# Kernel tuning notes

Measured on AMD Instinct MI355X. Metric: run time of the kernel, lower is better.

The kernel has to match this reference:

```python
import jax, jax.numpy as jnp
import numpy as np

B, N, D, NS, ITERS = 32, 2048, 512, 8, 3
EPS = 1e-8
SCALE = D ** -0.5
LN_EPS = 1e-5


def _ln(x, g, b):
    m = x.mean(-1, keepdims=True)
    v = ((x - m) ** 2).mean(-1, keepdims=True)
    return (x - m) * jax.lax.rsqrt(v + LN_EPS) * g + b


def setup_inputs() -> dict:
    key = jax.random.key(0)
    ks = iter(jax.random.split(key, 40))
    w = lambda *s: jax.random.normal(next(ks), s, jnp.float32) * 0.02
    inp = {
        'inputs': jax.random.normal(next(ks), (B, N, D), jnp.float32),
        'slot_noise': jax.random.normal(next(ks), (B, NS, D), jnp.float32),
        'slots_mu': jax.random.normal(next(ks), (1, 1, D), jnp.float32),
        'slots_logsigma': w(1, 1, D),
        'k_w': w(D, D), 'k_b': jnp.zeros((D,), jnp.float32),
        'v_w': w(D, D), 'v_b': jnp.zeros((D,), jnp.float32),
        'gru_w_ih': w(3 * D, D), 'gru_w_hh': w(3 * D, D),
        'gru_b_ih': jnp.zeros((3 * D,), jnp.float32),
        'gru_b_hh': jnp.zeros((3 * D,), jnp.float32),
        'ln_in_g': jnp.ones((D,), jnp.float32), 'ln_in_b': jnp.zeros((D,), jnp.float32),
        'ln_slots_g': jnp.ones((D,), jnp.float32), 'ln_slots_b': jnp.zeros((D,), jnp.float32),
        'ln_pre_g': jnp.ones((D,), jnp.float32), 'ln_pre_b': jnp.zeros((D,), jnp.float32),
        'mlp1_w': w(1024, D), 'mlp1_b': jnp.zeros((1024,), jnp.float32),
        'mlp2_w': w(1024, 1024), 'mlp2_b': jnp.zeros((1024,), jnp.float32),
        'mlp3_w': w(512, 1024), 'mlp3_b': jnp.zeros((512,), jnp.float32),
        'mlp4_w': w(256, 512), 'mlp4_b': jnp.zeros((256,), jnp.float32),
    }
    return inp


def reference(inputs, slot_noise, slots_mu, slots_logsigma, k_w, k_b, v_w, v_b,
              gru_w_ih, gru_w_hh, gru_b_ih, gru_b_hh,
              ln_in_g, ln_in_b, ln_slots_g, ln_slots_b, ln_pre_g, ln_pre_b,
              mlp1_w, mlp1_b, mlp2_w, mlp2_b, mlp3_w, mlp3_b, mlp4_w, mlp4_b):
    b, n, d = inputs.shape
    # stochastic slot init: mu + exp(logsigma) * noise  -> [b, ns, d]
    slots = slots_mu + jnp.exp(slots_logsigma) * slot_noise
    x = _ln(inputs, ln_in_g, ln_in_b)
    k = x @ k_w.T + k_b
    v = x @ v_w.T + v_b
    updates = slots
    for _ in range(ITERS):
        slots_prev = slots
        q = _ln(slots, ln_slots_g, ln_slots_b)
        dots = jnp.einsum('bid,bjd->bij', q, k) * SCALE  # [b, ns, n]
        attn = jax.nn.softmax(dots, axis=1) + EPS        # softmax over slot axis
        attn = attn / attn.sum(-1, keepdims=True)        # renorm over tokens
        updates = jnp.einsum('bjd,bij->bid', v, attn)    # [b, ns, d]
        # GRUCell(updates, slots_prev), then residual add of updates
        u = updates.reshape(-1, d)
        h = slots_prev.reshape(-1, d)
        gi = u @ gru_w_ih.T + gru_b_ih
        gh = h @ gru_w_hh.T + gru_b_hh
        i_r, i_z, i_n = jnp.split(gi, 3, axis=-1)
        h_r, h_z, h_n = jnp.split(gh, 3, axis=-1)
        r = jax.nn.sigmoid(i_r + h_r)
        z = jax.nn.sigmoid(i_z + h_z)
        nn_ = jnp.tanh(i_n + r * h_n)
        h_new = (1.0 - z) * nn_ + z * h
        slots = (u + h_new).reshape(b, -1, d)
    # output MLP with exact GELU (torch default)
    s = _ln(slots, ln_pre_g, ln_pre_b)
    s = jax.nn.gelu(s @ mlp1_w.T + mlp1_b, approximate=False)
    s = jax.nn.gelu(s @ mlp2_w.T + mlp2_b, approximate=False)
    s = jax.nn.gelu(s @ mlp3_w.T + mlp3_b, approximate=False)
    s = s @ mlp4_w.T + mlp4_b
    return (updates, s)
```

## Files before the change

### kernel.cpp

```cpp
#include <hip/hip_runtime.h>
#include <math.h>

#define Bb 32
#define Nn 2048
#define Dd 512
#define NS 8
#define ITERS 3
#define EPSf 1e-8f
#define SCALEf 0.04419417382415922f
#define LN_EPSf 1e-5f

#define QHS 520
#define PTS 136

typedef _Float16 half8 __attribute__((ext_vector_type(8)));
typedef float f32x4 __attribute__((ext_vector_type(4)));

__device__ __forceinline__ float waveReduceSum(float v) {
    #pragma unroll
    for (int m = 32; m >= 1; m >>= 1) v += __shfl_xor(v, m);
    return v;
}

__device__ __forceinline__ float gelu_exact(float x) {
    return 0.5f * x * (1.0f + erff(x * 0.7071067811865476f));
}

__device__ __forceinline__ void async_copy16(const _Float16* g, _Float16* l) {
    __builtin_amdgcn_global_load_lds(
        (const __attribute__((address_space(1))) unsigned int*)g,
        (__attribute__((address_space(3))) unsigned int*)l, 16, 0, 0);
}

__global__ __launch_bounds__(256) void megapack_kernel(
    const float* __restrict__ k_w, const float* __restrict__ v_w,
    const float* __restrict__ w_ih, const float* __restrict__ w_hh,
    const float* __restrict__ m1, const float* __restrict__ m2,
    const float* __restrict__ m3, const float* __restrict__ m4,
    _Float16* __restrict__ Bkv, _Float16* __restrict__ Bih, _Float16* __restrict__ Bhh,
    _Float16* __restrict__ Bm1, _Float16* __restrict__ Bm2,
    _Float16* __restrict__ Bm3, _Float16* __restrict__ Bm4) {
    int bid = blockIdx.x, tid = threadIdx.x;
    const float* src; _Float16* dst; int kbits, base;
    if (bid < 2048) {
        int i = bid * 256 + tid;
        Bkv[i] = (_Float16)(i < 262144 ? k_w[i] : v_w[i - 262144]);
        return;
    }
    else if (bid < 5120)  { src = w_ih; dst = Bih; kbits = 9;  base = 2048; }
    else if (bid < 8192)  { src = w_hh; dst = Bhh; kbits = 9;  base = 5120; }
    else if (bid < 10240) { src = m1;   dst = Bm1; kbits = 9;  base = 8192; }
    else if (bid < 14336) { src = m2;   dst = Bm2; kbits = 10; base = 10240; }
    else if (bid < 16384) { src = m3;   dst = Bm3; kbits = 10; base = 14336; }
    else                  { src = m4;   dst = Bm4; kbits = 9;  base = 16384; }
    int e = (bid - base) * 256 + tid;
    int K = 1 << kbits;
    int row = e >> kbits, k = e & (K - 1);
    _Float16 h = (_Float16)src[e];
    _Float16* d = dst + ((size_t)row << (kbits + 1));
    d[k] = h;
    d[K + k] = h;
}

__global__ __launch_bounds__(256) void pack_ln_single_kernel(
    const float* __restrict__ x, const float* __restrict__ g, const float* __restrict__ b,
    _Float16* __restrict__ Ap) {
    int wid = blockIdx.x * 4 + (threadIdx.x >> 6);
    int lane = threadIdx.x & 63;
    const float* row = x + (size_t)wid * Dd;
    float v[8];
    float s = 0.f, sq = 0.f;
    #pragma unroll
    for (int t = 0; t < 8; ++t) {
        v[t] = row[t * 64 + lane];
        s += v[t]; sq += v[t] * v[t];
    }
    s = waveReduceSum(s);
    sq = waveReduceSum(sq);
    float m = s * (1.0f / Dd);
    float var = sq * (1.0f / Dd) - m * m;
    float rs = rsqrtf(var + LN_EPSf);
    _Float16* outp = Ap + (size_t)wid * Dd;
    #pragma unroll
    for (int t = 0; t < 8; ++t) {
        int d = t * 64 + lane;
        outp[d] = (_Float16)((v[t] - m) * rs * g[d] + b[d]);
    }
}

__global__ __launch_bounds__(256) void slots_init_kernel(
    const float* __restrict__ noise, const float* __restrict__ mu,
    const float* __restrict__ ls, float* __restrict__ slots, _Float16* __restrict__ A2) {
    int idx = blockIdx.x * 256 + threadIdx.x;
    if (idx >= Bb * NS * Dd) return;
    int d = idx & (Dd - 1);
    float val = mu[d] + expf(ls[d]) * noise[idx];
    slots[idx] = val;
    int row = idx >> 9;
    _Float16 hi = (_Float16)val;
    A2[(size_t)(256 + row) * 1024 + d] = hi;
    A2[(size_t)(256 + row) * 1024 + 512 + d] = (_Float16)(val - (float)hi);
}

__device__ __forceinline__ void hgemm128_core(
    const _Float16* __restrict__ A, const _Float16* __restrict__ Bw,
    int K2, f32x4 acc[4][4], _Float16* As, _Float16* Bs) {
    const int tid = threadIdx.x;
    const int w = tid >> 6, lane = tid & 63;
    const int r8 = lane >> 3, seg = lane & 7;
    const int lr = lane & 15, quad = lane >> 4;
    const int wm = w >> 1, wn = w & 1;
    for (int k0 = 0; k0 < K2; k0 += 64) {
        __syncthreads();
        #pragma unroll
        for (int g = 0; g < 4; ++g) {
            int grp = w * 4 + g;
            int row = grp * 8 + r8;
            async_copy16(A + (size_t)row * K2 + k0 + seg * 8, As + grp * 512);
            async_copy16(Bw + (size_t)row * K2 + k0 + seg * 8, Bs + grp * 512);
        }
        __syncthreads();
        #pragma unroll
        for (int kk = 0; kk < 2; ++kk) {
            half8 a[4], b[4];
            #pragma unroll
            for (int t = 0; t < 4; ++t) {
                a[t] = *(const half8*)(As + (wm * 64 + t * 16 + lr) * 64 + kk * 32 + quad * 8);
                b[t] = *(const half8*)(Bs + (wn * 64 + t * 16 + lr) * 64 + kk * 32 + quad * 8);
            }
            #pragma unroll
            for (int mt = 0; mt < 4; ++mt)
                #pragma unroll
                for (int nt = 0; nt < 4; ++nt)
                    acc[mt][nt] = __builtin_amdgcn_mfma_f32_16x16x32_f16(
                        a[mt], b[nt], acc[mt][nt], 0, 0, 0);
        }
    }
}

__global__ __launch_bounds__(256) void kv_hgemm_kernel(
    const _Float16* __restrict__ Apack, const _Float16* __restrict__ Bkv,
    const float* __restrict__ k_b, const float* __restrict__ v_b,
    _Float16* __restrict__ khalf, _Float16* __restrict__ vT) {
    __shared__ _Float16 smem[17408];
    _Float16* As = smem;
    _Float16* Bs = smem + 8192;
    const int m0 = blockIdx.y * 128, n0 = blockIdx.x * 128;
    f32x4 acc[4][4];
    #pragma unroll
    for (int i = 0; i < 4; ++i)
        #pragma unroll
        for (int j = 0; j < 4; ++j) acc[i][j] = (f32x4){0.f, 0.f, 0.f, 0.f};
    hgemm128_core(Apack + (size_t)m0 * 512, Bkv + (size_t)n0 * 512, 512, acc, As, Bs);
    __syncthreads();
    const int tid = threadIdx.x;
    const int w = tid >> 6, lane = tid & 63;
    const int lr = lane & 15, quad = lane >> 4;
    const int wm = w >> 1, wn = w & 1;
    const bool isK = (n0 < 512);
    #pragma unroll
    for (int mt = 0; mt < 4; ++mt)
        #pragma unroll
        for (int nt = 0; nt < 4; ++nt) {
            int ml = wm * 64 + mt * 16 + quad * 4;
            int nl = wn * 64 + nt * 16 + lr;
            float bv = isK ? k_b[n0 + nl] : v_b[n0 - 512 + nl];
            #pragma unroll
            for (int r = 0; r < 4; ++r) {
                _Float16 h = (_Float16)(acc[mt][nt][r] + bv);
                if (isK) smem[(ml + r) * 136 + nl] = h;
                else     smem[nl * 136 + ml + r] = h;
            }
        }
    __syncthreads();
    int r = tid >> 1, half = tid & 1;
    _Float16* dst;
    if (isK) {
        dst = khalf + (size_t)(m0 + r) * 512 + n0 + half * 64;
    } else {
        int b = m0 >> 11, j0 = m0 & 2047, d0 = n0 - 512;
        dst = vT + ((size_t)b * 512 + d0 + r) * 2048 + j0 + half * 64;
    }
    #pragma unroll
    for (int c = 0; c < 8; ++c)
        *(half8*)(dst + c * 8) = *(const half8*)(smem + r * 136 + half * 64 + c * 8);
}

__global__ __launch_bounds__(256) void attn_kernel(
    const float* __restrict__ slots, const float* __restrict__ ln_g, const float* __restrict__ ln_b,
    const _Float16* __restrict__ khalf, const _Float16* __restrict__ vT,
    float* __restrict__ rawp, float* __restrict__ sumsp) {
    const int b = blockIdx.y, chunk = blockIdx.x;
    __shared__ _Float16 qh[16 * QHS];
    __shared__ _Float16 pT[16 * PTS];
    __shared__ float sums_lds[64];
    const int tid = threadIdx.x, w = tid >> 6, lane = tid & 63;
    const int lr = lane & 15, quad = lane >> 4;

    #pragma unroll
    for (int rr = 0; rr < 2; ++rr) {
        int row = w * 2 + rr;
        const float* sr = slots + ((size_t)b * NS + row) * Dd;
        float v[8]; float s = 0.f, sq = 0.f;
        #pragma unroll
        for (int t = 0; t < 8; ++t) {
            v[t] = sr[t * 64 + lane];
            s += v[t]; sq += v[t] * v[t];
        }
        s = waveReduceSum(s);
        sq = waveReduceSum(sq);
        float m = s * (1.0f / Dd);
        float var = sq * (1.0f / Dd) - m * m;
        float rs = rsqrtf(var + LN_EPSf);
        #pragma unroll
        for (int t = 0; t < 8; ++t) {
            int d = t * 64 + lane;
            qh[row * QHS + d] = (_Float16)(((v[t] - m) * rs * ln_g[d] + ln_b[d]) * SCALEf);
            qh[(row + 8) * QHS + d] = (_Float16)0.f;
        }
    }
    __syncthreads();

    const int j0 = chunk * 128 + w * 32;
    f32x4 dots[2];
    dots[0] = (f32x4){0.f, 0.f, 0.f, 0.f};
    dots[1] = (f32x4){0.f, 0.f, 0.f, 0.f};
    for (int ks = 0; ks < 16; ++ks) {
        half8 bq = *(const half8*)(qh + lr * QHS + ks * 32 + quad * 8);
        #pragma unroll
        for (int mf = 0; mf < 2; ++mf) {
            half8 ak = *(const half8*)(khalf + ((size_t)b * Nn + j0 + mf * 16 + lr) * 512 + ks * 32 + quad * 8);
            dots[mf] = __builtin_amdgcn_mfma_f32_16x16x32_f16(ak, bq, dots[mf], 0, 0, 0);
        }
    }
    float ssum = 0.f;
    #pragma unroll
    for (int mf = 0; mf < 2; ++mf) {
        f32x4 d = dots[mf];
        f32x4 mx = d;
        #pragma unroll
        for (int msk = 1; msk <= 4; msk <<= 1) {
            #pragma unroll
            for (int r = 0; r < 4; ++r) mx[r] = fmaxf(mx[r], __shfl_xor(mx[r], msk));
        }
        f32x4 p;
        #pragma unroll
        for (int r = 0; r < 4; ++r) p[r] = __expf(d[r] - mx[r]);
        f32x4 sm = p;
        #pragma unroll
        for (int msk = 1; msk <= 4; msk <<= 1) {
            #pragma unroll
            for (int r = 0; r < 4; ++r) sm[r] += __shfl_xor(sm[r], msk);
        }
        #pragma unroll
        for (int r = 0; r < 4; ++r) {
            _Float16 ph = (_Float16)(p[r] / sm[r] + EPSf);
            pT[lr * PTS + w * 32 + mf * 16 + quad * 4 + r] = ph;
            ssum += (float)ph;
        }
    }
    ssum += __shfl_xor(ssum, 16);
    ssum += __shfl_xor(ssum, 32);
    if (lane < 16) sums_lds[w * 16 + lane] = ssum;
    __syncthreads();

    f32x4 acc[8];
    #pragma unroll
    for (int nf = 0; nf < 8; ++nf) acc[nf] = (f32x4){0.f, 0.f, 0.f, 0.f};
    #pragma unroll
    for (int kc = 0; kc < 4; ++kc) {
        half8 ap = *(const half8*)(pT + lr * PTS + kc * 32 + quad * 8);
        #pragma unroll
        for (int nf = 0; nf < 8; ++nf) {
            int dcol = w * 128 + nf * 16 + lr;
            half8 bv = *(const half8*)(vT + ((size_t)b * 512 + dcol) * 2048 + chunk * 128 + kc * 32 + quad * 8);
            acc[nf] = __builtin_amdgcn_mfma_f32_16x16x32_f16(ap, bv, acc[nf], 0, 0, 0);
        }
    }
    if (quad < 2) {
        #pragma unroll
        for (int nf = 0; nf < 8; ++nf) {
            #pragma unroll
            for (int r = 0; r < 4; ++r) {
                int slot = quad * 4 + r;
                rawp[(((size_t)chunk * Bb + b) * NS + slot) * Dd + w * 128 + nf * 16 + lr] = acc[nf][r];
            }
        }
    }
    if (w == 0 && lane < NS) {
        float tot = sums_lds[lane] + sums_lds[16 + lane] + sums_lds[32 + lane] + sums_lds[48 + lane];
        sumsp[((size_t)chunk * Bb + b) * NS + lane] = tot;
    }
}

__global__ __launch_bounds__(256) void finalize_kernel(
    const float* __restrict__ rawp, const float* __restrict__ sumsp,
    float* __restrict__ u, float* __restrict__ out0, _Float16* __restrict__ A2) {
    int idx = blockIdx.x * 256 + threadIdx.x;
    int row = idx >> 9, k = idx & 511;
    float rs = 0.f, ss = 0.f;
    #pragma unroll
    for (int c = 0; c < 16; ++c) {
        rs += rawp[(size_t)c * 131072 + idx];
        ss += sumsp[c * 256 + row];
    }
    float val = rs / ss;
    u[idx] = val;
    out0[idx] = val;
    _Float16 hi = (_Float16)val;
    A2[(size_t)row * 1024 + k] = hi;
    A2[(size_t)row * 1024 + 512 + k] = (_Float16)(val - (float)hi);
}

__device__ __forceinline__ void hgemm64_core(
    const _Float16* __restrict__ A, const _Float16* __restrict__ Bw,
    int K2, f32x4 acc[2][2], _Float16* As, _Float16* Bs) {
    const int tid = threadIdx.x;
    const int w = tid >> 6, lane = tid & 63;
    const int r8 = lane >> 3, seg = lane & 7;
    const int lr = lane & 15, quad = lane >> 4;
    const int wm = w >> 1, wn = w & 1;
    for (int k0 = 0; k0 < K2; k0 += 64) {
        __syncthreads();
        #pragma unroll
        for (int p = 0; p < 2; ++p) {
            int grp = p * 4 + w;
            int row = grp * 8 + r8;
            async_copy16(A + (size_t)row * K2 + k0 + seg * 8, As + grp * 512);
            async_copy16(Bw + (size_t)row * K2 + k0 + seg * 8, Bs + grp * 512);
        }
        __syncthreads();
        #pragma unroll
        for (int kk = 0; kk < 2; ++kk) {
            half8 a[2], b[2];
            #pragma unroll
            for (int t = 0; t < 2; ++t) {
                a[t] = *(const half8*)(As + (wm * 32 + t * 16 + lr) * 64 + kk * 32 + quad * 8);
                b[t] = *(const half8*)(Bs + (wn * 32 + t * 16 + lr) * 64 + kk * 32 + quad * 8);
            }
            #pragma unroll
            for (int mt = 0; mt < 2; ++mt)
                #pragma unroll
                for (int nt = 0; nt < 2; ++nt)
                    acc[mt][nt] = __builtin_amdgcn_mfma_f32_16x16x32_f16(
                        a[mt], b[nt], acc[mt][nt], 0, 0, 0);
        }
    }
}

template <int ACT, int PACK>
__global__ __launch_bounds__(256) void hgemm64_kernel(
    const _Float16* __restrict__ A, const _Float16* __restrict__ Bw,
    const float* __restrict__ bias, float* __restrict__ C, _Float16* __restrict__ P,
    int K2, int N, int Kp) {
    __shared__ _Float16 As[4096], Bs[4096];
    const int m0 = blockIdx.y * 64, n0 = blockIdx.x * 64;
    f32x4 acc[2][2];
    #pragma unroll
    for (int i = 0; i < 2; ++i)
        #pragma unroll
        for (int j = 0; j < 2; ++j) acc[i][j] = (f32x4){0.f, 0.f, 0.f, 0.f};
    hgemm64_core(A + (size_t)m0 * K2, Bw + (size_t)n0 * K2, K2, acc, As, Bs);
    const int tid = threadIdx.x;
    const int w = tid >> 6, lane = tid & 63;
    const int lr = lane & 15, quad = lane >> 4;
    const int wm = w >> 1, wn = w & 1;
    #pragma unroll
    for (int mt = 0; mt < 2; ++mt)
        #pragma unroll
        for (int nt = 0; nt < 2; ++nt) {
            int n = n0 + wn * 32 + nt * 16 + lr;
            float bv = bias[n];
            #pragma unroll
            for (int r = 0; r < 4; ++r) {
                int m = m0 + wm * 32 + mt * 16 + quad * 4 + r;
                float val = acc[mt][nt][r] + bv;
                if (ACT) val = gelu_exact(val);
                if (PACK) {
                    _Float16 hi = (_Float16)val;
                    P[(size_t)m * 2 * Kp + n] = hi;
                    P[(size_t)m * 2 * Kp + Kp + n] = (_Float16)(val - (float)hi);
                } else {
                    C[(size_t)m * N + n] = val;
                }
            }
        }
}

__global__ __launch_bounds__(256) void gru_gemm_kernel(
    const _Float16* __restrict__ A2, const _Float16* __restrict__ Bih,
    const _Float16* __restrict__ Bhh, const float* __restrict__ b_ih,
    const float* __restrict__ b_hh, float* __restrict__ gi, float* __restrict__ gh) {
    __shared__ _Float16 As[4096], Bs[4096];
    const int by = blockIdx.y;
    const int n0 = blockIdx.x * 64;
    const _Float16* Ap; const _Float16* Bw; const float* bias; float* C;
    if (by < 4) { Ap = A2 + (size_t)by * 64 * 1024;        Bw = Bih; bias = b_ih; C = gi + (size_t)by * 64 * 1536; }
    else        { Ap = A2 + (size_t)(256 + (by - 4) * 64) * 1024; Bw = Bhh; bias = b_hh; C = gh + (size_t)(by - 4) * 64 * 1536; }
    f32x4 acc[2][2];
    #pragma unroll
    for (int i = 0; i < 2; ++i)
        #pragma unroll
        for (int j = 0; j < 2; ++j) acc[i][j] = (f32x4){0.f, 0.f, 0.f, 0.f};
    hgemm64_core(Ap, Bw + (size_t)n0 * 1024, 1024, acc, As, Bs);
    const int tid = threadIdx.x;
    const int w = tid >> 6, lane = tid & 63;
    const int lr = lane & 15, quad = lane >> 4;
    const int wm = w >> 1, wn = w & 1;
    #pragma unroll
    for (int mt = 0; mt < 2; ++mt)
        #pragma unroll
        for (int nt = 0; nt < 2; ++nt) {
            int n = n0 + wn * 32 + nt * 16 + lr;
            float bv = bias[n];
            #pragma unroll
            for (int r = 0; r < 4; ++r) {
                int m = wm * 32 + mt * 16 + quad * 4 + r;
                C[(size_t)m * 1536 + n] = acc[mt][nt][r] + bv;
            }
        }
}

__global__ __launch_bounds__(256) void gru_elem_kernel(
    const float* __restrict__ gi, const float* __restrict__ gh,
    const float* __restrict__ u, float* __restrict__ slots, _Float16* __restrict__ A2) {
    int idx = blockIdx.x * 256 + threadIdx.x;
    if (idx >= Bb * NS * Dd) return;
    int row = idx >> 9, d = idx & (Dd - 1);
    const float* gir = gi + (size_t)row * 1536;
    const float* ghr = gh + (size_t)row * 1536;
    float ir = gir[d], iz = gir[512 + d], in_ = gir[1024 + d];
    float hr = ghr[d], hz = ghr[512 + d], hn = ghr[1024 + d];
    float r = 1.0f / (1.0f + expf(-(ir + hr)));
    float z = 1.0f / (1.0f + expf(-(iz + hz)));
    float n = tanhf(in_ + r * hn);
    float h = slots[idx];
    float hnew = (1.0f - z) * n + z * h;
    float val = u[idx] + hnew;
    slots[idx] = val;
    _Float16 hi = (_Float16)val;
    A2[(size_t)(256 + row) * 1024 + d] = hi;
    A2[(size_t)(256 + row) * 1024 + 512 + d] = (_Float16)(val - (float)hi);
}

__global__ __launch_bounds__(256) void lnpack_kernel(
    const float* __restrict__ x, const float* __restrict__ g, const float* __restrict__ b,
    _Float16* __restrict__ P) {
    int wid = blockIdx.x * 4 + (threadIdx.x >> 6);
    int lane = threadIdx.x & 63;
    const float* row = x + (size_t)wid * Dd;
    float v[8];
    float s = 0.f, sq = 0.f;
    #pragma unroll
    for (int t = 0; t < 8; ++t) {
        v[t] = row[t * 64 + lane];
        s += v[t]; sq += v[t] * v[t];
    }
    s = waveReduceSum(s);
    sq = waveReduceSum(sq);
    float m = s * (1.0f / Dd);
    float var = sq * (1.0f / Dd) - m * m;
    float rs = rsqrtf(var + LN_EPSf);
    _Float16* outp = P + (size_t)wid * 1024;
    #pragma unroll
    for (int t = 0; t < 8; ++t) {
        int d = t * 64 + lane;
        float a = (v[t] - m) * rs * g[d] + b[d];
        _Float16 hi = (_Float16)a;
        outp[d] = hi;
        outp[512 + d] = (_Float16)(a - (float)hi);
    }
}

extern "C" void kernel_launch(void* const* d_in, const int* in_sizes, int n_in,
                              void* d_out, int out_size, void* d_ws, size_t ws_size,
                              hipStream_t stream) {
    const float* inputs   = (const float*)d_in[0];
    const float* noise    = (const float*)d_in[1];
    const float* mu       = (const float*)d_in[2];
    const float* lsig     = (const float*)d_in[3];
    const float* k_w      = (const float*)d_in[4];
    const float* k_b      = (const float*)d_in[5];
    const float* v_w      = (const float*)d_in[6];
    const float* v_b      = (const float*)d_in[7];
    const float* w_ih     = (const float*)d_in[8];
    const float* w_hh     = (const float*)d_in[9];
    const float* b_ih     = (const float*)d_in[10];
    const float* b_hh     = (const float*)d_in[11];
    const float* ln_in_g  = (const float*)d_in[12];
    const float* ln_in_b  = (const float*)d_in[13];
    const float* ln_s_g   = (const float*)d_in[14];
    const float* ln_s_b   = (const float*)d_in[15];
    const float* ln_p_g   = (const float*)d_in[16];
    const float* ln_p_b   = (const float*)d_in[17];
    const float* mlp1_w   = (const float*)d_in[18];
    const float* mlp1_b   = (const float*)d_in[19];
    const float* mlp2_w   = (const float*)d_in[20];
    const float* mlp2_b   = (const float*)d_in[21];
    const float* mlp3_w   = (const float*)d_in[22];
    const float* mlp3_b   = (const float*)d_in[23];
    const float* mlp4_w   = (const float*)d_in[24];
    const float* mlp4_b   = (const float*)d_in[25];
    float* out0 = (float*)d_out;
    float* out1 = (float*)d_out + Bb * NS * Dd;

    char* wp = (char*)d_ws;
    auto alloc = [&](size_t bytes) -> void* {
        void* p = (void*)wp;
        wp += (bytes + 255) & ~(size_t)255;
        return p;
    };
    const size_t MR = (size_t)Bb * Nn;
    _Float16* Apack = (_Float16*)alloc(MR * 512 * 2);
    _Float16* khalf = (_Float16*)alloc(MR * 512 * 2);
    _Float16* vT    = (_Float16*)alloc((size_t)Bb * 512 * Nn * 2);
    _Float16* Bkv   = (_Float16*)alloc((size_t)1024 * 512 * 2);
    _Float16* Bih   = (_Float16*)alloc((size_t)1536 * 1024 * 2);
    _Float16* Bhh   = (_Float16*)alloc((size_t)1536 * 1024 * 2);
    _Float16* Bm1   = (_Float16*)alloc((size_t)1024 * 1024 * 2);
    _Float16* Bm2   = (_Float16*)alloc((size_t)1024 * 2048 * 2);
    _Float16* Bm3   = (_Float16*)alloc((size_t)512 * 2048 * 2);
    _Float16* Bm4   = (_Float16*)alloc((size_t)256 * 1024 * 2);
    float* slots    = (float*)alloc((size_t)Bb * NS * Dd * 4);
    float* rawp     = (float*)alloc((size_t)16 * Bb * NS * Dd * 4);
    float* sumsp    = (float*)alloc((size_t)16 * Bb * NS * 4);
    float* ubuf     = (float*)alloc((size_t)Bb * NS * Dd * 4);
    float* gi       = (float*)alloc((size_t)Bb * NS * 1536 * 4);
    float* gh       = (float*)alloc((size_t)Bb * NS * 1536 * 4);
    _Float16* A2    = (_Float16*)alloc((size_t)512 * 1024 * 2);
    _Float16* P1    = (_Float16*)alloc((size_t)256 * 1024 * 2);
    _Float16* P2    = (_Float16*)alloc((size_t)256 * 2048 * 2);
    _Float16* P3    = (_Float16*)alloc((size_t)256 * 2048 * 2);
    _Float16* P4    = (_Float16*)alloc((size_t)256 * 1024 * 2);

    megapack_kernel<<<16896, 256, 0, stream>>>(
        k_w, v_w, w_ih, w_hh, mlp1_w, mlp2_w, mlp3_w, mlp4_w,
        Bkv, Bih, Bhh, Bm1, Bm2, Bm3, Bm4);
    pack_ln_single_kernel<<<MR / 4, 256, 0, stream>>>(inputs, ln_in_g, ln_in_b, Apack);
    slots_init_kernel<<<(Bb * NS * Dd) / 256, 256, 0, stream>>>(noise, mu, lsig, slots, A2);

    kv_hgemm_kernel<<<dim3(8, MR / 128), 256, 0, stream>>>(Apack, Bkv, k_b, v_b, khalf, vT);

    for (int it = 0; it < ITERS; ++it) {
        attn_kernel<<<dim3(16, Bb), 256, 0, stream>>>(slots, ln_s_g, ln_s_b, khalf, vT, rawp, sumsp);
        finalize_kernel<<<512, 256, 0, stream>>>(rawp, sumsp, ubuf, out0, A2);
        gru_gemm_kernel<<<dim3(24, 8), 256, 0, stream>>>(A2, Bih, Bhh, b_ih, b_hh, gi, gh);
        gru_elem_kernel<<<512, 256, 0, stream>>>(gi, gh, ubuf, slots, A2);
    }

    lnpack_kernel<<<64, 256, 0, stream>>>(slots, ln_p_g, ln_p_b, P1);
    hgemm64_kernel<1, 1><<<dim3(16, 4), 256, 0, stream>>>(P1, Bm1, mlp1_b, nullptr, P2, 1024, 1024, 1024);
    hgemm64_kernel<1, 1><<<dim3(16, 4), 256, 0, stream>>>(P2, Bm2, mlp2_b, nullptr, P3, 2048, 1024, 1024);
    hgemm64_kernel<1, 1><<<dim3(8, 4), 256, 0, stream>>>(P3, Bm3, mlp3_b, nullptr, P4, 2048, 512, 512);
    hgemm64_kernel<0, 0><<<dim3(4, 4), 256, 0, stream>>>(P4, Bm4, mlp4_b, out1, nullptr, 1024, 256, 256);
}
```

Baseline: 664.4 us.

## Split attention into more chunks, swizzle KV GEMM grid, vectorize LN, fuse final LN

The attention kernel now processes 64 tokens per block over 32 chunks instead of 128 over 16. This doubles the grid to raise occupancy, at the cost of twice as many partial sums for finalize to reduce. The KV projection GEMM uses a 1D grid with a swizzled tile order to improve L2 reuse of the A rows across the eight N tiles. The input layernorm pack uses float4 loads and 16-byte half8 stores with a contiguous per-lane mapping. The final pre-MLP layernorm is folded into the last GRU elementwise kernel, which is now one row per wave, removing a separate launch.

```diff
diff --git a/kernel.cpp b/kernel.cpp
--- a/kernel.cpp
+++ b/kernel.cpp
@@ -11,9 +11,11 @@
 #define LN_EPSf 1e-5f
 
 #define QHS 520
-#define PTS 136
+#define PTS 72
+#define CHUNKS 32
 
 typedef _Float16 half8 __attribute__((ext_vector_type(8)));
+typedef _Float16 half4 __attribute__((ext_vector_type(4)));
 typedef float f32x4 __attribute__((ext_vector_type(4)));
 
 __device__ __forceinline__ float waveReduceSum(float v) {
@@ -67,25 +69,27 @@
     _Float16* __restrict__ Ap) {
     int wid = blockIdx.x * 4 + (threadIdx.x >> 6);
     int lane = threadIdx.x & 63;
-    const float* row = x + (size_t)wid * Dd;
-    float v[8];
+    const float4* row4 = (const float4*)(x + (size_t)wid * Dd);
+    float4 va = row4[lane * 2], vb = row4[lane * 2 + 1];
+    float v[8] = {va.x, va.y, va.z, va.w, vb.x, vb.y, vb.z, vb.w};
     float s = 0.f, sq = 0.f;
     #pragma unroll
-    for (int t = 0; t < 8; ++t) {
-        v[t] = row[t * 64 + lane];
-        s += v[t]; sq += v[t] * v[t];
-    }
+    for (int t = 0; t < 8; ++t) { s += v[t]; sq += v[t] * v[t]; }
     s = waveReduceSum(s);
     sq = waveReduceSum(sq);
     float m = s * (1.0f / Dd);
     float var = sq * (1.0f / Dd) - m * m;
     float rs = rsqrtf(var + LN_EPSf);
-    _Float16* outp = Ap + (size_t)wid * Dd;
-    #pragma unroll
-    for (int t = 0; t < 8; ++t) {
-        int d = t * 64 + lane;
-        outp[d] = (_Float16)((v[t] - m) * rs * g[d] + b[d]);
-    }
+    const float4* g4 = (const float4*)g;
+    const float4* b4 = (const float4*)b;
+    float4 ga = g4[lane * 2], gb = g4[lane * 2 + 1];
+    float4 ba = b4[lane * 2], bb = b4[lane * 2 + 1];
+    float gg[8] = {ga.x, ga.y, ga.z, ga.w, gb.x, gb.y, gb.z, gb.w};
+    float bbv[8] = {ba.x, ba.y, ba.z, ba.w, bb.x, bb.y, bb.z, bb.w};
+    half8 o;
+    #pragma unroll
+    for (int t = 0; t < 8; ++t) o[t] = (_Float16)((v[t] - m) * rs * gg[t] + bbv[t]);
+    *(half8*)(Ap + (size_t)wid * Dd + lane * 8) = o;
 }
 
 __global__ __launch_bounds__(256) void slots_init_kernel(
@@ -145,7 +149,9 @@
     __shared__ _Float16 smem[17408];
     _Float16* As = smem;
     _Float16* Bs = smem + 8192;
-    const int m0 = blockIdx.y * 128, n0 = blockIdx.x * 128;
+    const int f = blockIdx.x;
+    const int m0 = ((f & 7) + ((f >> 6) << 3)) * 128;
+    const int n0 = ((f >> 3) & 7) * 128;
     f32x4 acc[4][4];
     #pragma unroll
     for (int i = 0; i < 4; ++i)
@@ -221,22 +227,16 @@
     }
     __syncthreads();
 
-    const int j0 = chunk * 128 + w * 32;
-    f32x4 dots[2];
-    dots[0] = (f32x4){0.f, 0.f, 0.f, 0.f};
-    dots[1] = (f32x4){0.f, 0.f, 0.f, 0.f};
+    const int j0 = chunk * 64 + w * 16;
+    f32x4 dots = (f32x4){0.f, 0.f, 0.f, 0.f};
     for (int ks = 0; ks < 16; ++ks) {
         half8 bq = *(const half8*)(qh + lr * QHS + ks * 32 + quad * 8);
-        #pragma unroll
-        for (int mf = 0; mf < 2; ++mf) {
-            half8 ak = *(const half8*)(khalf + ((size_t)b * Nn + j0 + mf * 16 + lr) * 512 + ks * 32 + quad * 8);
-            dots[mf] = __builtin_amdgcn_mfma_f32_16x16x32_f16(ak, bq, dots[mf], 0, 0, 0);
-        }
+        half8 ak = *(const half8*)(khalf + ((size_t)b * Nn + j0 + lr) * 512 + ks * 32 + quad * 8);
+        dots = __builtin_amdgcn_mfma_f32_16x16x32_f16(ak, bq, dots, 0, 0, 0);
     }
     float ssum = 0.f;
-    #pragma unroll
-    for (int mf = 0; mf < 2; ++mf) {
-        f32x4 d = dots[mf];
+    {
+        f32x4 d = dots;
         f32x4 mx = d;
         #pragma unroll
         for (int msk = 1; msk <= 4; msk <<= 1) {
@@ -255,7 +255,7 @@
         #pragma unroll
         for (int r = 0; r < 4; ++r) {
             _Float16 ph = (_Float16)(p[r] / sm[r] + EPSf);
-            pT[lr * PTS + w * 32 + mf * 16 + quad * 4 + r] = ph;
+            pT[lr * PTS + w * 16 + quad * 4 + r] = ph;
             ssum += (float)ph;
         }
     }
@@ -268,12 +268,12 @@
     #pragma unroll
     for (int nf = 0; nf < 8; ++nf) acc[nf] = (f32x4){0.f, 0.f, 0.f, 0.f};
     #pragma unroll
-    for (int kc = 0; kc < 4; ++kc) {
+    for (int kc = 0; kc < 2; ++kc) {
         half8 ap = *(const half8*)(pT + lr * PTS + kc * 32 + quad * 8);
         #pragma unroll
         for (int nf = 0; nf < 8; ++nf) {
             int dcol = w * 128 + nf * 16 + lr;
-            half8 bv = *(const half8*)(vT + ((size_t)b * 512 + dcol) * 2048 + chunk * 128 + kc * 32 + quad * 8);
+            half8 bv = *(const half8*)(vT + ((size_t)b * 512 + dcol) * 2048 + chunk * 64 + kc * 32 + quad * 8);
             acc[nf] = __builtin_amdgcn_mfma_f32_16x16x32_f16(ap, bv, acc[nf], 0, 0, 0);
         }
     }
@@ -300,7 +300,7 @@
     int row = idx >> 9, k = idx & 511;
     float rs = 0.f, ss = 0.f;
     #pragma unroll
-    for (int c = 0; c < 16; ++c) {
+    for (int c = 0; c < CHUNKS; ++c) {
         rs += rawp[(size_t)c * 131072 + idx];
         ss += sumsp[c * 256 + row];
     }
@@ -423,52 +423,48 @@
 
 __global__ __launch_bounds__(256) void gru_elem_kernel(
     const float* __restrict__ gi, const float* __restrict__ gh,
-    const float* __restrict__ u, float* __restrict__ slots, _Float16* __restrict__ A2) {
-    int idx = blockIdx.x * 256 + threadIdx.x;
-    if (idx >= Bb * NS * Dd) return;
-    int row = idx >> 9, d = idx & (Dd - 1);
+    const float* __restrict__ u, float* __restrict__ slots, _Float16* __restrict__ A2,
+    const float* __restrict__ lnp_g, const float* __restrict__ lnp_b,
+    _Float16* __restrict__ P1, int last) {
+    int row = blockIdx.x * 4 + (threadIdx.x >> 6);
+    int lane = threadIdx.x & 63;
     const float* gir = gi + (size_t)row * 1536;
     const float* ghr = gh + (size_t)row * 1536;
-    float ir = gir[d], iz = gir[512 + d], in_ = gir[1024 + d];
-    float hr = ghr[d], hz = ghr[512 + d], hn = ghr[1024 + d];
-    float r = 1.0f / (1.0f + expf(-(ir + hr)));
-    float z = 1.0f / (1.0f + expf(-(iz + hz)));
-    float n = tanhf(in_ + r * hn);
-    float h = slots[idx];
-    float hnew = (1.0f - z) * n + z * h;
-    float val = u[idx] + hnew;
-    slots[idx] = val;
-    _Float16 hi = (_Float16)val;
-    A2[(size_t)(256 + row) * 1024 + d] = hi;
-    A2[(size_t)(256 + row) * 1024 + 512 + d] = (_Float16)(val - (float)hi);
-}
-
-__global__ __launch_bounds__(256) void lnpack_kernel(
-    const float* __restrict__ x, const float* __restrict__ g, const float* __restrict__ b,
-    _Float16* __restrict__ P) {
-    int wid = blockIdx.x * 4 + (threadIdx.x >> 6);
-    int lane = threadIdx.x & 63;
-    const float* row = x + (size_t)wid * Dd;
-    float v[8];
-    float s = 0.f, sq = 0.f;
-    #pragma unroll
-    for (int t = 0; t < 8; ++t) {
-        v[t] = row[t * 64 + lane];
-        s += v[t]; sq += v[t] * v[t];
-    }
-    s = waveReduceSum(s);
-    sq = waveReduceSum(sq);
-    float m = s * (1.0f / Dd);
-    float var = sq * (1.0f / Dd) - m * m;
-    float rs = rsqrtf(var + LN_EPSf);
-    _Float16* outp = P + (size_t)wid * 1024;
+    float val[8];
     #pragma unroll
     for (int t = 0; t < 8; ++t) {
         int d = t * 64 + lane;
-        float a = (v[t] - m) * rs * g[d] + b[d];
-        _Float16 hi = (_Float16)a;
-        outp[d] = hi;
-        outp[512 + d] = (_Float16)(a - (float)hi);
+        float ir = gir[d], iz = gir[512 + d], in_ = gir[1024 + d];
+        float hr = ghr[d], hz = ghr[512 + d], hn = ghr[1024 + d];
+        float r = 1.0f / (1.0f + expf(-(ir + hr)));
+        float z = 1.0f / (1.0f + expf(-(iz + hz)));
+        float n = tanhf(in_ + r * hn);
+        float h = slots[(size_t)row * 512 + d];
+        float hnew = (1.0f - z) * n + z * h;
+        float vv = u[(size_t)row * 512 + d] + hnew;
+        val[t] = vv;
+        slots[(size_t)row * 512 + d] = vv;
+        _Float16 hi = (_Float16)vv;
+        A2[(size_t)(256 + row) * 1024 + d] = hi;
+        A2[(size_t)(256 + row) * 1024 + 512 + d] = (_Float16)(vv - (float)hi);
+    }
+    if (last) {
+        float s = 0.f, sq = 0.f;
+        #pragma unroll
+        for (int t = 0; t < 8; ++t) { s += val[t]; sq += val[t] * val[t]; }
+        s = waveReduceSum(s);
+        sq = waveReduceSum(sq);
+        float m = s * (1.0f / Dd);
+        float var = sq * (1.0f / Dd) - m * m;
+        float rs = rsqrtf(var + LN_EPSf);
+        #pragma unroll
+        for (int t = 0; t < 8; ++t) {
+            int d = t * 64 + lane;
+            float a = (val[t] - m) * rs * lnp_g[d] + lnp_b[d];
+            _Float16 hi = (_Float16)a;
+            P1[(size_t)row * 1024 + d] = hi;
+            P1[(size_t)row * 1024 + 512 + d] = (_Float16)(a - (float)hi);
+        }
     }
 }
 
@@ -522,8 +518,8 @@
     _Float16* Bm3   = (_Float16*)alloc((size_t)512 * 2048 * 2);
     _Float16* Bm4   = (_Float16*)alloc((size_t)256 * 1024 * 2);
     float* slots    = (float*)alloc((size_t)Bb * NS * Dd * 4);
-    float* rawp     = (float*)alloc((size_t)16 * Bb * NS * Dd * 4);
-    float* sumsp    = (float*)alloc((size_t)16 * Bb * NS * 4);
+    float* rawp     = (float*)alloc((size_t)CHUNKS * Bb * NS * Dd * 4);
+    float* sumsp    = (float*)alloc((size_t)CHUNKS * Bb * NS * 4);
     float* ubuf     = (float*)alloc((size_t)Bb * NS * Dd * 4);
     float* gi       = (float*)alloc((size_t)Bb * NS * 1536 * 4);
     float* gh       = (float*)alloc((size_t)Bb * NS * 1536 * 4);
@@ -539,16 +535,16 @@
     pack_ln_single_kernel<<<MR / 4, 256, 0, stream>>>(inputs, ln_in_g, ln_in_b, Apack);
     slots_init_kernel<<<(Bb * NS * Dd) / 256, 256, 0, stream>>>(noise, mu, lsig, slots, A2);
 
-    kv_hgemm_kernel<<<dim3(8, MR / 128), 256, 0, stream>>>(Apack, Bkv, k_b, v_b, khalf, vT);
+    kv_hgemm_kernel<<<4096, 256, 0, stream>>>(Apack, Bkv, k_b, v_b, khalf, vT);
 
     for (int it = 0; it < ITERS; ++it) {
-        attn_kernel<<<dim3(16, Bb), 256, 0, stream>>>(slots, ln_s_g, ln_s_b, khalf, vT, rawp, sumsp);
+        attn_kernel<<<dim3(CHUNKS, Bb), 256, 0, stream>>>(slots, ln_s_g, ln_s_b, khalf, vT, rawp, sumsp);
         finalize_kernel<<<512, 256, 0, stream>>>(rawp, sumsp, ubuf, out0, A2);
         gru_gemm_kernel<<<dim3(24, 8), 256, 0, stream>>>(A2, Bih, Bhh, b_ih, b_hh, gi, gh);
-        gru_elem_kernel<<<512, 256, 0, stream>>>(gi, gh, ubuf, slots, A2);
-    }
-
-    lnpack_kernel<<<64, 256, 0, stream>>>(slots, ln_p_g, ln_p_b, P1);
+        gru_elem_kernel<<<64, 256, 0, stream>>>(gi, gh, ubuf, slots, A2,
+                                                ln_p_g, ln_p_b, P1, it == ITERS - 1 ? 1 : 0);
+    }
+
     hgemm64_kernel<1, 1><<<dim3(16, 4), 256, 0, stream>>>(P1, Bm1, mlp1_b, nullptr, P2, 1024, 1024, 1024);
     hgemm64_kernel<1, 1><<<dim3(16, 4), 256, 0, stream>>>(P2, Bm2, mlp2_b, nullptr, P3, 2048, 1024, 1024);
     hgemm64_kernel<1, 1><<<dim3(8, 4), 256, 0, stream>>>(P3, Bm3, mlp3_b, nullptr, P4, 2048, 512, 512);
```

After: 681.4 us. +2.6%, slower.
